# Performance work log

Hardware: AMD Instinct MI355X
Metric: run time of the kernel (lower is better)

Reference implementation:

```python
import jax, jax.numpy as jnp
import numpy as np

KS = 3          # deformable kernel size
PAD = 1         # padding (kernel_size // 2)
EPS = 1e-5      # BatchNorm eps


def conv2d(x, w, b):
    # plain 3x3 conv, stride 1, pad 1, NCHW / OIHW
    y = jax.lax.conv_general_dilated(x, w, window_strides=(1, 1),
                                     padding=[(PAD, PAD), (PAD, PAD)],
                                     dimension_numbers=("NCHW", "OIHW", "NCHW"))
    return y + b[None, :, None, None]


def deform_conv(x, offset, mask, w, b):
    # modulated deformable conv v2 (torchvision deform_conv2d semantics)
    B, C, H, W = x.shape
    K = KS * KS
    ky, kx = jnp.meshgrid(jnp.arange(KS), jnp.arange(KS), indexing="ij")
    ky = ky.reshape(-1).astype(x.dtype)
    kx = kx.reshape(-1).astype(x.dtype)
    off = offset.reshape(B, K, 2, H, W)          # channel order: (dy, dx) per kernel tap
    dy, dx = off[:, :, 0], off[:, :, 1]          # [B,K,H,W]
    py = dy + (ky - PAD)[None, :, None, None] + jnp.arange(H, dtype=x.dtype)[None, None, :, None]
    px = dx + (kx - PAD)[None, :, None, None] + jnp.arange(W, dtype=x.dtype)[None, None, None, :]
    y0 = jnp.floor(py); x0 = jnp.floor(px)
    ly = py - y0; lx = px - x0
    y0i = y0.astype(jnp.int32); x0i = x0.astype(jnp.int32)
    y1i = y0i + 1; x1i = x0i + 1
    xf = x.reshape(B, C, H * W)

    def gather(yi, xi):
        valid = (yi >= 0) & (yi < H) & (xi >= 0) & (xi < W)          # zero padding outside
        idx = jnp.clip(yi, 0, H - 1) * W + jnp.clip(xi, 0, W - 1)    # [B,K,H,W]
        g = jax.vmap(lambda xb, ib: jnp.take(xb, ib, axis=1))(xf, idx.reshape(B, -1))
        g = g.reshape(B, C, K, H, W)
        return g * valid[:, None].astype(x.dtype)

    v = (gather(y0i, x0i) * ((1 - ly) * (1 - lx))[:, None]
         + gather(y0i, x1i) * ((1 - ly) * lx)[:, None]
         + gather(y1i, x0i) * (ly * (1 - lx))[:, None]
         + gather(y1i, x1i) * (ly * lx)[:, None])                    # [B,C,K,H,W]
    v = v * mask[:, None]                                            # modulation
    out = jnp.einsum("bckhw,ock->bohw", v, w.reshape(w.shape[0], C, K))
    return out + b[None, :, None, None]


def setup_inputs() -> dict:
    key = jax.random.key(0)
    ks = jax.random.split(key, 5)
    B, Cin, Cout, H, W = 8, 64, 64, 128, 128
    K = KS * KS
    x = jax.random.normal(ks[0], (B, Cin, H, W), jnp.float32)
    off_w = jax.random.normal(ks[1], (2 * K, Cin, KS, KS), jnp.float32) * 0.01
    off_b = jnp.zeros((2 * K,), jnp.float32)
    mod_w = jax.random.normal(ks[2], (K, Cin, KS, KS), jnp.float32) * 0.01
    mod_b = jnp.zeros((K,), jnp.float32)
    w = jax.random.normal(ks[3], (Cout, Cin, KS, KS), jnp.float32) * (1.0 / np.sqrt(Cin * K))
    b = jnp.zeros((Cout,), jnp.float32)
    gamma = jnp.ones((Cout,), jnp.float32)
    beta = jnp.zeros((Cout,), jnp.float32)
    return {"x": x, "off_w": off_w, "off_b": off_b, "mod_w": mod_w,
            "mod_b": mod_b, "w": w, "b": b, "gamma": gamma, "beta": beta}


def reference(x, off_w, off_b, mod_w, mod_b, w, b, gamma, beta):
    offset = conv2d(x, off_w, off_b)                       # [B,2K,H,W]
    mask = 2.0 * jax.nn.sigmoid(conv2d(x, mod_w, mod_b))   # [B,K,H,W]
    y = deform_conv(x, offset, mask, w, b)                 # [B,Cout,H,W]
    # BatchNorm2d (training-mode batch stats, biased variance)
    mean = y.mean(axis=(0, 2, 3), keepdims=True)
    var = y.var(axis=(0, 2, 3), keepdims=True)
    yn = (y - mean) / jnp.sqrt(var + EPS)
    yn = gamma[None, :, None, None] * yn + beta[None, :, None, None]
    return jax.nn.relu(yn)
```

## Files before the change

### kernel.cpp

```cpp
#include <hip/hip_runtime.h>
#include <math.h>

#define Hn 128
#define Wn 128
#define HW 16384
#define NPIX 131072
#define EPSv 1e-5f

#define XT_OFF   0
#define OFF_OFF  4194304
#define MASK_OFF 6553600
#define WBTA_OFF 7733248
#define WBTB_OFF 7743488
#define STAT_OFF 7763968


typedef short s16x8 __attribute__((ext_vector_type(8)));
typedef unsigned short u16x4 __attribute__((ext_vector_type(4)));
typedef float f32x4 __attribute__((ext_vector_type(4)));

__device__ __forceinline__ unsigned short f2bf(float f) {
  unsigned u = __float_as_uint(f);
  return (unsigned short)((u + 0x7fffu + ((u >> 16) & 1u)) >> 16);
}
__device__ __forceinline__ float bf2f(unsigned short s) {
  return __uint_as_float((unsigned)s << 16);
}

__global__ __launch_bounds__(256) void prep_kernel(
    const float* __restrict__ off_w, const float* __restrict__ mod_w,
    const float* __restrict__ w, unsigned short* __restrict__ wbtA,
    unsigned short* __restrict__ wbtB, float* __restrict__ stat) {
  int i = blockIdx.x * 256 + threadIdx.x;
  if (i < 128) stat[i] = 0.f;
  if (i < 20480) {
    int e = i & 31, oc = (i >> 5) & 31, it = i >> 10;
    int tp = it % 5, chunk = it / 5;
    int tap = tp * 2 + (e >> 4);
    int c = (chunk << 4) + (e & 15);
    float v = 0.f;
    if (tap < 9) {
      if (oc < 18) v = off_w[(oc * 64 + c) * 9 + tap];
      else if (oc < 27) v = mod_w[((oc - 18) * 64 + c) * 9 + tap];
    }
    wbtA[i] = f2bf(v);
  } else if (i < 20480 + 40960) {
    int j = i - 20480;
    int j3 = j & 7;
    int l = (j >> 3) & 63;
    int nt = (j >> 9) & 3;
    int it = j >> 11;
    int tp = it % 5, chunk = it / 5;
    int tap = tp * 2 + (l >> 5);
    int c = (chunk << 4) + (((l >> 4) & 1) << 3) + j3;
    int oc = (nt << 4) + (l & 15);
    float v = (tap < 9) ? w[(oc * 64 + c) * 9 + tap] : 0.f;
    wbtB[j] = f2bf(v);
  }
}

__global__ __launch_bounds__(256) void xform_kernel(
    const float* __restrict__ x, unsigned short* __restrict__ xt) {
  int blk = blockIdx.x;
  int b = blk & 7;
  int hw = ((blk >> 3) << 8) + threadIdx.x;
  const float* xb = x + ((size_t)(b << 6) << 14) + hw;
  unsigned short* o = xt + (((size_t)(b << 14)) + hw) * 64;
#pragma unroll
  for (int g = 0; g < 8; ++g) {
    float v[8];
#pragma unroll
    for (int j = 0; j < 8; ++j) v[j] = xb[(size_t)((g << 3) + j) << 14];
    s16x8 pk;
#pragma unroll
    for (int j = 0; j < 8; ++j) pk[j] = (short)f2bf(v[j]);
    *(s16x8*)(o + (g << 3)) = pk;
  }
}

__global__ __launch_bounds__(256, 4) void convA_mfma_kernel(
    const unsigned short* __restrict__ xt, const unsigned short* __restrict__ wbtA,
    const float* __restrict__ off_b, const float* __restrict__ mod_b,
    float* __restrict__ off_out, float* __restrict__ mask_out) {
  int t = threadIdx.x;
  int bx = blockIdx.x;
  int b = bx & 7, h = bx >> 3;
  int ln = t & 15, quad = (t >> 4) & 3, wv = t >> 6;
  int p0 = (wv << 5) + ln, p1 = p0 + 16;
  int s_ = quad >> 1, cj = (quad & 1) << 3;

  f32x4 acc[2][2];
#pragma unroll
  for (int mt = 0; mt < 2; ++mt)
#pragma unroll
    for (int nt = 0; nt < 2; ++nt) acc[mt][nt] = (f32x4){0.f, 0.f, 0.f, 0.f};

  const unsigned short* xtb = xt + ((size_t)(b << 14)) * 64;

#pragma unroll 5
  for (int it = 0; it < 20; ++it) {
    int chunk = it / 5, tp = it - chunk * 5;
    int tap = tp * 2 + s_;
    s16x8 B0 = (s16x8){0, 0, 0, 0, 0, 0, 0, 0};
    s16x8 B1 = (s16x8){0, 0, 0, 0, 0, 0, 0, 0};
    if (tap < 9) {
      int gy = h + tap / 3 - 1;
      if (gy >= 0 && gy < Hn) {
        const unsigned short* rowp = xtb + ((size_t)(gy << 7)) * 64 + (chunk << 4) + cj;
        int gx0 = p0 + tap % 3 - 1;
        int gx1 = p1 + tap % 3 - 1;
        if (gx0 >= 0 && gx0 < Wn) B0 = *(const s16x8*)(rowp + (gx0 << 6));
        if (gx1 >= 0 && gx1 < Wn) B1 = *(const s16x8*)(rowp + (gx1 << 6));
      }
    }
#pragma unroll
    for (int mt = 0; mt < 2; ++mt) {
      s16x8 A = *(const s16x8*)(wbtA + (size_t)((it << 5) + (mt << 4) + ln) * 32 + (quad << 3));
      acc[mt][0] = __builtin_amdgcn_mfma_f32_16x16x32_bf16(A, B0, acc[mt][0], 0, 0, 0);
      acc[mt][1] = __builtin_amdgcn_mfma_f32_16x16x32_bf16(A, B1, acc[mt][1], 0, 0, 0);
    }
  }

  int hw = h << 7;
#pragma unroll
  for (int mt = 0; mt < 2; ++mt)
#pragma unroll
    for (int r = 0; r < 4; ++r) {
      int oc = (mt << 4) + (quad << 2) + r;
#pragma unroll
      for (int nt = 0; nt < 2; ++nt) {
        int px = (wv << 5) + (nt << 4) + ln;
        float val = acc[mt][nt][r];
        if (oc < 18) {
          off_out[(((size_t)b * 18 + oc) << 14) + hw + px] = val + off_b[oc];
        } else if (oc < 27) {
          float z = val + mod_b[oc - 18];
          mask_out[(((size_t)b * 9 + (oc - 18)) << 14) + hw + px] = 2.f / (1.f + expf(-z));
        }
      }
    }
}

__global__ __launch_bounds__(256, 4) void deform_mfma_kernel(
    const unsigned short* __restrict__ xt, const float* __restrict__ off,
    const float* __restrict__ mask, const unsigned short* __restrict__ wbtB,
    const float* __restrict__ bias, float* __restrict__ y) {
  __shared__ unsigned short geow[9 * 128 * 4];
  __shared__ unsigned short geoi[9 * 128];
  int t = threadIdx.x;
  int bx = blockIdx.x;
  int b = bx & 7, h = bx >> 3;
  int lane = t & 63, wv = t >> 6;
  int l4 = lane & 15;
  int s4 = lane >> 4;
  int tapS = lane >> 5;
  int chalf = s4 & 1;
  int hw = h << 7;

  for (int i = t; i < 1152; i += 256) {
    int tap = i >> 7, p2 = i & 127;
    int ob = ((b * 18 + 2 * tap) << 14) + hw + p2;
    float dy = off[ob];
    float dx = off[ob + HW];
    float m = mask[((b * 9 + tap) << 14) + hw + p2];
    float py = dy + (float)(h + tap / 3 - 1);
    float pxf = dx + (float)(p2 + tap % 3 - 1);
    float y0f = floorf(py), x0f = floorf(pxf);
    float ly = py - y0f, lx = pxf - x0f;
    int y0 = (int)y0f, x0 = (int)x0f;
    int y1 = y0 + 1, x1 = x0 + 1;
    float fy0 = (y0 >= 0 && y0 < Hn) ? 1.f : 0.f;
    float fy1 = (y1 >= 0 && y1 < Hn) ? 1.f : 0.f;
    float fx0 = (x0 >= 0 && x0 < Wn) ? 1.f : 0.f;
    float fx1 = (x1 >= 0 && x1 < Wn) ? 1.f : 0.f;
    float ax0 = (1.f - lx) * fx0, ax1 = lx * fx1;
    float ay0 = (1.f - ly) * fy0 * m, ay1 = ly * fy1 * m;
    int cy0 = min(max(y0, 0), Hn - 1), cy1 = min(max(y1, 0), Hn - 1);
    int cx0 = min(max(x0, 0), Wn - 1), cx1 = min(max(x1, 0), Wn - 1);
    int cbase = min(cx0, Wn - 2), rbase = min(cy0, Hn - 2);
    float gx0 = (cx0 == cbase ? ax0 : 0.f) + (cx1 == cbase ? ax1 : 0.f);
    float gx1 = (cx0 == cbase + 1 ? ax0 : 0.f) + (cx1 == cbase + 1 ? ax1 : 0.f);
    float gy0 = (cy0 == rbase ? ay0 : 0.f) + (cy1 == rbase ? ay1 : 0.f);
    float gy1 = (cy0 == rbase + 1 ? ay0 : 0.f) + (cy1 == rbase + 1 ? ay1 : 0.f);
    unsigned short* gw = geow + i * 4;
    gw[0] = f2bf(gy0);
    gw[1] = f2bf(gy1);
    gw[2] = f2bf(gx0);
    gw[3] = f2bf(gx1);
    geoi[i] = (unsigned short)((rbase << 7) + cbase);
  }
  __syncthreads();

  f32x4 acc[2][4];
#pragma unroll
  for (int m = 0; m < 2; ++m)
#pragma unroll
    for (int n = 0; n < 4; ++n) acc[m][n] = (f32x4){0.f, 0.f, 0.f, 0.f};

  const unsigned short* xtb = xt + ((size_t)(b << 14)) * 64;

  for (int tp = 0; tp < 5; ++tp) {
    int tap = tp * 2 + tapS;
    bool live = (tap < 9);
    float gy0[2], gy1[2], gx0[2], gx1[2];
    const unsigned short* cpb[2];
#pragma unroll
    for (int m = 0; m < 2; ++m) {
      if (live) {
        int px = (wv << 5) + (m << 4) + l4;
        int gidx = (tap << 7) + px;
        u16x4 wq = *(const u16x4*)(geow + gidx * 4);
        unsigned ib = geoi[gidx];
        gy0[m] = bf2f(wq[0]);
        gy1[m] = bf2f(wq[1]);
        gx0[m] = bf2f(wq[2]);
        gx1[m] = bf2f(wq[3]);
        cpb[m] = xtb + (size_t)ib * 64 + (chalf << 3);
      } else {
        cpb[m] = xtb;
        gy0[m] = gy1[m] = gx0[m] = gx1[m] = 0.f;
      }
    }
#pragma unroll 2
    for (int chunk = 0; chunk < 4; ++chunk) {
      int it = chunk * 5 + tp;
      s16x8 A[2];
#pragma unroll
      for (int m = 0; m < 2; ++m) {
        if (live) {
          const unsigned short* cp = cpb[m] + (chunk << 4);
          s16x8 c00 = *(const s16x8*)(cp);
          s16x8 c01 = *(const s16x8*)(cp + 64);
          s16x8 c10 = *(const s16x8*)(cp + 8192);
          s16x8 c11 = *(const s16x8*)(cp + 8192 + 64);
#pragma unroll
          for (int j = 0; j < 8; ++j) {
            float v = gy0[m] * (gx0[m] * bf2f((unsigned short)c00[j]) +
                                gx1[m] * bf2f((unsigned short)c01[j])) +
                      gy1[m] * (gx0[m] * bf2f((unsigned short)c10[j]) +
                                gx1[m] * bf2f((unsigned short)c11[j]));
            A[m][j] = (short)f2bf(v);
          }
        } else {
#pragma unroll
          for (int j = 0; j < 8; ++j) A[m][j] = 0;
        }
      }
      const unsigned short* wb = wbtB + (((size_t)it) << 11) + (lane << 3);
#pragma unroll
      for (int n = 0; n < 4; ++n) {
        s16x8 Bf = *(const s16x8*)(wb + (n << 9));
        acc[0][n] = __builtin_amdgcn_mfma_f32_16x16x32_bf16(A[0], Bf, acc[0][n], 0, 0, 0);
        acc[1][n] = __builtin_amdgcn_mfma_f32_16x16x32_bf16(A[1], Bf, acc[1][n], 0, 0, 0);
      }
    }
  }

#pragma unroll
  for (int m = 0; m < 2; ++m) {
    int px0 = (wv << 5) + (m << 4) + (s4 << 2);
#pragma unroll
    for (int n = 0; n < 4; ++n) {
      int oc = (n << 4) + l4;
      float bv = bias[oc];
      float4 o;
      o.x = acc[m][n][0] + bv;
      o.y = acc[m][n][1] + bv;
      o.z = acc[m][n][2] + bv;
      o.w = acc[m][n][3] + bv;
      *(float4*)(y + (((size_t)(b << 6) + oc) << 14) + hw + px0) = o;
    }
  }
}

__global__ __launch_bounds__(256) void stats2_kernel(
    const float* __restrict__ y, float* __restrict__ stat) {
  int bxx = blockIdx.x;
  int c = bxx & 63, sl = bxx >> 6;
  int bb = sl >> 1;
  const float4* yp = (const float4*)(y + (((size_t)bb * 64 + c) << 14) + ((sl & 1) << 13));
  float s = 0.f, ss = 0.f;
  for (int i = threadIdx.x; i < 2048; i += 256) {
    float4 v = yp[i];
    s += v.x + v.y + v.z + v.w;
    ss += v.x * v.x + v.y * v.y + v.z * v.z + v.w * v.w;
  }
#pragma unroll
  for (int o = 32; o > 0; o >>= 1) {
    s += __shfl_xor(s, o);
    ss += __shfl_xor(ss, o);
  }
  __shared__ float shs[4], shss[4];
  int lane = threadIdx.x & 63, wv = threadIdx.x >> 6;
  if (lane == 0) { shs[wv] = s; shss[wv] = ss; }
  __syncthreads();
  if (threadIdx.x == 0) {
    float S = shs[0] + shs[1] + shs[2] + shs[3];
    float SS = shss[0] + shss[1] + shss[2] + shss[3];
    atomicAdd(stat + c, S);
    atomicAdd(stat + 64 + c, SS);
  }
}

__global__ __launch_bounds__(256) void bnrelu_kernel(
    float* __restrict__ y, const float* __restrict__ stat,
    const float* __restrict__ gamma, const float* __restrict__ beta) {
  float4* y4 = (float4*)y;
  for (int i = blockIdx.x * 256 + threadIdx.x; i < 2097152; i += gridDim.x * 256) {
    int c = (i >> 12) & 63;
    float mean = stat[c] * (1.f / (float)NPIX);
    float var = stat[64 + c] * (1.f / (float)NPIX) - mean * mean;
    float r = rsqrtf(var + EPSv);
    float g = gamma[c] * r;
    float bt = beta[c] - mean * g;
    float4 v = y4[i];
    v.x = fmaxf(v.x * g + bt, 0.f);
    v.y = fmaxf(v.y * g + bt, 0.f);
    v.z = fmaxf(v.z * g + bt, 0.f);
    v.w = fmaxf(v.w * g + bt, 0.f);
    y4[i] = v;
  }
}

extern "C" void kernel_launch(void* const* d_in, const int* in_sizes, int n_in,
                              void* d_out, int out_size, void* d_ws, size_t ws_size,
                              hipStream_t stream) {
  const float* x     = (const float*)d_in[0];
  const float* off_w = (const float*)d_in[1];
  const float* off_b = (const float*)d_in[2];
  const float* mod_w = (const float*)d_in[3];
  const float* mod_b = (const float*)d_in[4];
  const float* w     = (const float*)d_in[5];
  const float* b     = (const float*)d_in[6];
  const float* gamma = (const float*)d_in[7];
  const float* beta  = (const float*)d_in[8];
  float* out = (float*)d_out;
  float* ws  = (float*)d_ws;

  unsigned short* xt  = (unsigned short*)(ws + XT_OFF);
  float* offo  = ws + OFF_OFF;
  float* masko = ws + MASK_OFF;
  unsigned short* wbtA = (unsigned short*)(ws + WBTA_OFF);
  unsigned short* wbtB = (unsigned short*)(ws + WBTB_OFF);
  float* stat  = ws + STAT_OFF;

  prep_kernel<<<240, 256, 0, stream>>>(off_w, mod_w, w, wbtA, wbtB, stat);
  xform_kernel<<<512, 256, 0, stream>>>(x, xt);
  convA_mfma_kernel<<<1024, 256, 0, stream>>>(xt, wbtA, off_b, mod_b, offo, masko);
  deform_mfma_kernel<<<1024, 256, 0, stream>>>(xt, offo, masko, wbtB, b, out);
  stats2_kernel<<<1024, 256, 0, stream>>>(out, stat);
  bnrelu_kernel<<<8192, 256, 0, stream>>>(out, stat, gamma, beta);
}
```

Measured before the change: 233.6 us.

## Split conv and deform kernels into half-row blocks and precombine bilinear weights

Both the offset/mask conv and the deformable conv kernels now cover half an image row per block. Each wave computes one 16-pixel tile instead of two, the grid doubles, and launch bounds ask for 8 waves per SIMD, which cuts register pressure and raises occupancy. The deform kernel also stores the four combined bilinear weights (gy*gx) in LDS and packs results with the hardware v_cvt_pk_bf16_f32 instruction, which reduces per-element ALU work. In exchange, A-operand reuse across two MFMA tiles is lost and the weights are loaded more often. Rounding the product weights to bf16 changes numerics slightly.

Measured after the change: 250.8 us. 7.4% more time.

```diff
diff --git a/kernel.cpp b/kernel.cpp
--- a/kernel.cpp
+++ b/kernel.cpp
@@ -18,6 +18,7 @@
 typedef short s16x8 __attribute__((ext_vector_type(8)));
 typedef unsigned short u16x4 __attribute__((ext_vector_type(4)));
 typedef float f32x4 __attribute__((ext_vector_type(4)));
+typedef unsigned int u32x4 __attribute__((ext_vector_type(4)));
 
 __device__ __forceinline__ unsigned short f2bf(float f) {
   unsigned u = __float_as_uint(f);
@@ -25,6 +26,11 @@
 }
 __device__ __forceinline__ float bf2f(unsigned short s) {
   return __uint_as_float((unsigned)s << 16);
+}
+__device__ __forceinline__ unsigned cvt_pk_bf16(float lo, float hi) {
+  unsigned r;
+  asm("v_cvt_pk_bf16_f32 %0, %1, %2" : "=v"(r) : "v"(lo), "v"(hi));
+  return r;
 }
 
 __global__ __launch_bounds__(256) void prep_kernel(
@@ -78,22 +84,20 @@
   }
 }
 
-__global__ __launch_bounds__(256, 4) void convA_mfma_kernel(
+__global__ __launch_bounds__(256, 8) void convA_mfma_kernel(
     const unsigned short* __restrict__ xt, const unsigned short* __restrict__ wbtA,
     const float* __restrict__ off_b, const float* __restrict__ mod_b,
     float* __restrict__ off_out, float* __restrict__ mask_out) {
   int t = threadIdx.x;
   int bx = blockIdx.x;
-  int b = bx & 7, h = bx >> 3;
+  int half = bx & 1, b = (bx >> 1) & 7, h = bx >> 4;
   int ln = t & 15, quad = (t >> 4) & 3, wv = t >> 6;
-  int p0 = (wv << 5) + ln, p1 = p0 + 16;
+  int p0 = (half << 6) + (wv << 4) + ln;
   int s_ = quad >> 1, cj = (quad & 1) << 3;
 
-  f32x4 acc[2][2];
-#pragma unroll
-  for (int mt = 0; mt < 2; ++mt)
-#pragma unroll
-    for (int nt = 0; nt < 2; ++nt) acc[mt][nt] = (f32x4){0.f, 0.f, 0.f, 0.f};
+  f32x4 acc[2];
+#pragma unroll
+  for (int mt = 0; mt < 2; ++mt) acc[mt] = (f32x4){0.f, 0.f, 0.f, 0.f};
 
   const unsigned short* xtb = xt + ((size_t)(b << 14)) * 64;
 
@@ -102,22 +106,18 @@
     int chunk = it / 5, tp = it - chunk * 5;
     int tap = tp * 2 + s_;
     s16x8 B0 = (s16x8){0, 0, 0, 0, 0, 0, 0, 0};
-    s16x8 B1 = (s16x8){0, 0, 0, 0, 0, 0, 0, 0};
     if (tap < 9) {
       int gy = h + tap / 3 - 1;
       if (gy >= 0 && gy < Hn) {
         const unsigned short* rowp = xtb + ((size_t)(gy << 7)) * 64 + (chunk << 4) + cj;
         int gx0 = p0 + tap % 3 - 1;
-        int gx1 = p1 + tap % 3 - 1;
         if (gx0 >= 0 && gx0 < Wn) B0 = *(const s16x8*)(rowp + (gx0 << 6));
-        if (gx1 >= 0 && gx1 < Wn) B1 = *(const s16x8*)(rowp + (gx1 << 6));
       }
     }
 #pragma unroll
     for (int mt = 0; mt < 2; ++mt) {
       s16x8 A = *(const s16x8*)(wbtA + (size_t)((it << 5) + (mt << 4) + ln) * 32 + (quad << 3));
-      acc[mt][0] = __builtin_amdgcn_mfma_f32_16x16x32_bf16(A, B0, acc[mt][0], 0, 0, 0);
-      acc[mt][1] = __builtin_amdgcn_mfma_f32_16x16x32_bf16(A, B1, acc[mt][1], 0, 0, 0);
+      acc[mt] = __builtin_amdgcn_mfma_f32_16x16x32_bf16(A, B0, acc[mt], 0, 0, 0);
     }
   }
 
@@ -127,44 +127,43 @@
 #pragma unroll
     for (int r = 0; r < 4; ++r) {
       int oc = (mt << 4) + (quad << 2) + r;
-#pragma unroll
-      for (int nt = 0; nt < 2; ++nt) {
-        int px = (wv << 5) + (nt << 4) + ln;
-        float val = acc[mt][nt][r];
-        if (oc < 18) {
-          off_out[(((size_t)b * 18 + oc) << 14) + hw + px] = val + off_b[oc];
-        } else if (oc < 27) {
-          float z = val + mod_b[oc - 18];
-          mask_out[(((size_t)b * 9 + (oc - 18)) << 14) + hw + px] = 2.f / (1.f + expf(-z));
-        }
+      int px = p0;
+      float val = acc[mt][r];
+      if (oc < 18) {
+        off_out[(((size_t)b * 18 + oc) << 14) + hw + px] = val + off_b[oc];
+      } else if (oc < 27) {
+        float z = val + mod_b[oc - 18];
+        mask_out[(((size_t)b * 9 + (oc - 18)) << 14) + hw + px] = 2.f / (1.f + expf(-z));
       }
     }
 }
 
-__global__ __launch_bounds__(256, 4) void deform_mfma_kernel(
+__global__ __launch_bounds__(256, 8) void deform_mfma_kernel(
     const unsigned short* __restrict__ xt, const float* __restrict__ off,
     const float* __restrict__ mask, const unsigned short* __restrict__ wbtB,
     const float* __restrict__ bias, float* __restrict__ y) {
-  __shared__ unsigned short geow[9 * 128 * 4];
-  __shared__ unsigned short geoi[9 * 128];
+  __shared__ unsigned short geow[9 * 64 * 4];
+  __shared__ unsigned short geoi[9 * 64];
   int t = threadIdx.x;
   int bx = blockIdx.x;
-  int b = bx & 7, h = bx >> 3;
+  int half = bx & 1, b = (bx >> 1) & 7, h = bx >> 4;
   int lane = t & 63, wv = t >> 6;
   int l4 = lane & 15;
   int s4 = lane >> 4;
   int tapS = lane >> 5;
   int chalf = s4 & 1;
   int hw = h << 7;
-
-  for (int i = t; i < 1152; i += 256) {
-    int tap = i >> 7, p2 = i & 127;
-    int ob = ((b * 18 + 2 * tap) << 14) + hw + p2;
+  int pxb = half << 6;
+
+  for (int i = t; i < 576; i += 256) {
+    int tap = i >> 6, p2 = i & 63;
+    int px = pxb + p2;
+    int ob = ((b * 18 + 2 * tap) << 14) + hw + px;
     float dy = off[ob];
     float dx = off[ob + HW];
-    float m = mask[((b * 9 + tap) << 14) + hw + p2];
+    float m = mask[((b * 9 + tap) << 14) + hw + px];
     float py = dy + (float)(h + tap / 3 - 1);
-    float pxf = dx + (float)(p2 + tap % 3 - 1);
+    float pxf = dx + (float)(px + tap % 3 - 1);
     float y0f = floorf(py), x0f = floorf(pxf);
     float ly = py - y0f, lx = pxf - x0f;
     int y0 = (int)y0f, x0 = (int)x0f;
@@ -183,93 +182,82 @@
     float gy0 = (cy0 == rbase ? ay0 : 0.f) + (cy1 == rbase ? ay1 : 0.f);
     float gy1 = (cy0 == rbase + 1 ? ay0 : 0.f) + (cy1 == rbase + 1 ? ay1 : 0.f);
     unsigned short* gw = geow + i * 4;
-    gw[0] = f2bf(gy0);
-    gw[1] = f2bf(gy1);
-    gw[2] = f2bf(gx0);
-    gw[3] = f2bf(gx1);
+    gw[0] = f2bf(gy0 * gx0);
+    gw[1] = f2bf(gy0 * gx1);
+    gw[2] = f2bf(gy1 * gx0);
+    gw[3] = f2bf(gy1 * gx1);
     geoi[i] = (unsigned short)((rbase << 7) + cbase);
   }
   __syncthreads();
 
-  f32x4 acc[2][4];
-#pragma unroll
-  for (int m = 0; m < 2; ++m)
-#pragma unroll
-    for (int n = 0; n < 4; ++n) acc[m][n] = (f32x4){0.f, 0.f, 0.f, 0.f};
+  f32x4 acc[4];
+#pragma unroll
+  for (int n = 0; n < 4; ++n) acc[n] = (f32x4){0.f, 0.f, 0.f, 0.f};
 
   const unsigned short* xtb = xt + ((size_t)(b << 14)) * 64;
 
   for (int tp = 0; tp < 5; ++tp) {
     int tap = tp * 2 + tapS;
     bool live = (tap < 9);
-    float gy0[2], gy1[2], gx0[2], gx1[2];
-    const unsigned short* cpb[2];
-#pragma unroll
-    for (int m = 0; m < 2; ++m) {
-      if (live) {
-        int px = (wv << 5) + (m << 4) + l4;
-        int gidx = (tap << 7) + px;
-        u16x4 wq = *(const u16x4*)(geow + gidx * 4);
-        unsigned ib = geoi[gidx];
-        gy0[m] = bf2f(wq[0]);
-        gy1[m] = bf2f(wq[1]);
-        gx0[m] = bf2f(wq[2]);
-        gx1[m] = bf2f(wq[3]);
-        cpb[m] = xtb + (size_t)ib * 64 + (chalf << 3);
-      } else {
-        cpb[m] = xtb;
-        gy0[m] = gy1[m] = gx0[m] = gx1[m] = 0.f;
-      }
-    }
-#pragma unroll 2
+    float w00, w01, w10, w11;
+    const unsigned short* cpb;
+    if (live) {
+      int gidx = (tap << 6) + (wv << 4) + l4;
+      u16x4 wq = *(const u16x4*)(geow + gidx * 4);
+      unsigned ib = geoi[gidx];
+      w00 = bf2f(wq[0]);
+      w01 = bf2f(wq[1]);
+      w10 = bf2f(wq[2]);
+      w11 = bf2f(wq[3]);
+      cpb = xtb + (size_t)ib * 64 + (chalf << 3);
+    } else {
+      cpb = xtb;
+      w00 = w01 = w10 = w11 = 0.f;
+    }
+#pragma unroll
     for (int chunk = 0; chunk < 4; ++chunk) {
       int it = chunk * 5 + tp;
-      s16x8 A[2];
-#pragma unroll
-      for (int m = 0; m < 2; ++m) {
-        if (live) {
-          const unsigned short* cp = cpb[m] + (chunk << 4);
-          s16x8 c00 = *(const s16x8*)(cp);
-          s16x8 c01 = *(const s16x8*)(cp + 64);
-          s16x8 c10 = *(const s16x8*)(cp + 8192);
-          s16x8 c11 = *(const s16x8*)(cp + 8192 + 64);
-#pragma unroll
-          for (int j = 0; j < 8; ++j) {
-            float v = gy0[m] * (gx0[m] * bf2f((unsigned short)c00[j]) +
-                                gx1[m] * bf2f((unsigned short)c01[j])) +
-                      gy1[m] * (gx0[m] * bf2f((unsigned short)c10[j]) +
-                                gx1[m] * bf2f((unsigned short)c11[j]));
-            A[m][j] = (short)f2bf(v);
-          }
-        } else {
-#pragma unroll
-          for (int j = 0; j < 8; ++j) A[m][j] = 0;
+      u32x4 au = (u32x4){0u, 0u, 0u, 0u};
+      if (live) {
+        const unsigned short* cp = cpb + (chunk << 4);
+        s16x8 c00 = *(const s16x8*)(cp);
+        s16x8 c01 = *(const s16x8*)(cp + 64);
+        s16x8 c10 = *(const s16x8*)(cp + 8192);
+        s16x8 c11 = *(const s16x8*)(cp + 8192 + 64);
+#pragma unroll
+        for (int jj = 0; jj < 4; ++jj) {
+          float v0 = w00 * bf2f((unsigned short)c00[2 * jj]) +
+                     w01 * bf2f((unsigned short)c01[2 * jj]) +
+                     w10 * bf2f((unsigned short)c10[2 * jj]) +
+                     w11 * bf2f((unsigned short)c11[2 * jj]);
+          float v1 = w00 * bf2f((unsigned short)c00[2 * jj + 1]) +
+                     w01 * bf2f((unsigned short)c01[2 * jj + 1]) +
+                     w10 * bf2f((unsigned short)c10[2 * jj + 1]) +
+                     w11 * bf2f((unsigned short)c11[2 * jj + 1]);
+          au[jj] = cvt_pk_bf16(v0, v1);
         }
       }
+      s16x8 A = __builtin_bit_cast(s16x8, au);
       const unsigned short* wb = wbtB + (((size_t)it) << 11) + (lane << 3);
 #pragma unroll
       for (int n = 0; n < 4; ++n) {
         s16x8 Bf = *(const s16x8*)(wb + (n << 9));
-        acc[0][n] = __builtin_amdgcn_mfma_f32_16x16x32_bf16(A[0], Bf, acc[0][n], 0, 0, 0);
-        acc[1][n] = __builtin_amdgcn_mfma_f32_16x16x32_bf16(A[1], Bf, acc[1][n], 0, 0, 0);
+        acc[n] = __builtin_amdgcn_mfma_f32_16x16x32_bf16(A, Bf, acc[n], 0, 0, 0);
       }
     }
   }
 
-#pragma unroll
-  for (int m = 0; m < 2; ++m) {
-    int px0 = (wv << 5) + (m << 4) + (s4 << 2);
-#pragma unroll
-    for (int n = 0; n < 4; ++n) {
-      int oc = (n << 4) + l4;
-      float bv = bias[oc];
-      float4 o;
-      o.x = acc[m][n][0] + bv;
-      o.y = acc[m][n][1] + bv;
-      o.z = acc[m][n][2] + bv;
-      o.w = acc[m][n][3] + bv;
-      *(float4*)(y + (((size_t)(b << 6) + oc) << 14) + hw + px0) = o;
-    }
+  int px0 = pxb + (wv << 4) + (s4 << 2);
+#pragma unroll
+  for (int n = 0; n < 4; ++n) {
+    int oc = (n << 4) + l4;
+    float bv = bias[oc];
+    float4 o;
+    o.x = acc[n][0] + bv;
+    o.y = acc[n][1] + bv;
+    o.z = acc[n][2] + bv;
+    o.w = acc[n][3] + bv;
+    *(float4*)(y + (((size_t)(b << 6) + oc) << 14) + hw + px0) = o;
   }
 }
 
@@ -346,8 +334,8 @@
 
   prep_kernel<<<240, 256, 0, stream>>>(off_w, mod_w, w, wbtA, wbtB, stat);
   xform_kernel<<<512, 256, 0, stream>>>(x, xt);
-  convA_mfma_kernel<<<1024, 256, 0, stream>>>(xt, wbtA, off_b, mod_b, offo, masko);
-  deform_mfma_kernel<<<1024, 256, 0, stream>>>(xt, offo, masko, wbtB, b, out);
+  convA_mfma_kernel<<<2048, 256, 0, stream>>>(xt, wbtA, off_b, mod_b, offo, masko);
+  deform_mfma_kernel<<<2048, 256, 0, stream>>>(xt, offo, masko, wbtB, b, out);
   stats2_kernel<<<1024, 256, 0, stream>>>(out, stat);
   bnrelu_kernel<<<8192, 256, 0, stream>>>(out, stat, gamma, beta);
 }
```

## Fuse offset/mask conv into deformable conv kernel via shared memory

Applied to the files above, without the earlier changes.

Merges the offset/mask convolution kernel into the deformable convolution kernel. Each block computes its row's offsets and sigmoid mask into shared memory, so the global write and re-read of the offset/mask tensors and one launch go away. It also precomputes the four combined bilinear weights per sample and packs the bf16 conversion with v_cvt_pk_bf16_f32, which cuts per-element ALU work in the gather loop. In exchange the fused kernel uses more shared memory (about 13.8KB extra) and more registers, which may lower occupancy, and folding the weights before the bf16 rounding slightly changes numerics.

After: 230.1 us. Within noise of the previous version (-1.5%).

```diff
diff --git a/kernel.cpp b/kernel.cpp
--- a/kernel.cpp
+++ b/kernel.cpp
@@ -8,16 +8,15 @@
 #define EPSv 1e-5f
 
 #define XT_OFF   0
-#define OFF_OFF  4194304
-#define MASK_OFF 6553600
-#define WBTA_OFF 7733248
-#define WBTB_OFF 7743488
-#define STAT_OFF 7763968
+#define WBTA_OFF 4194304
+#define WBTB_OFF 4204544
+#define STAT_OFF 4225024
 
 
 typedef short s16x8 __attribute__((ext_vector_type(8)));
 typedef unsigned short u16x4 __attribute__((ext_vector_type(4)));
 typedef float f32x4 __attribute__((ext_vector_type(4)));
+typedef unsigned int u32x4 __attribute__((ext_vector_type(4)));
 
 __device__ __forceinline__ unsigned short f2bf(float f) {
   unsigned u = __float_as_uint(f);
@@ -25,6 +24,11 @@
 }
 __device__ __forceinline__ float bf2f(unsigned short s) {
   return __uint_as_float((unsigned)s << 16);
+}
+__device__ __forceinline__ unsigned cvt_pk_bf16(float lo, float hi) {
+  unsigned r;
+  asm("v_cvt_pk_bf16_f32 %0, %1, %2" : "=v"(r) : "v"(lo), "v"(hi));
+  return r;
 }
 
 __global__ __launch_bounds__(256) void prep_kernel(
@@ -78,91 +82,81 @@
   }
 }
 
-__global__ __launch_bounds__(256, 4) void convA_mfma_kernel(
+__global__ __launch_bounds__(256, 4) void fused_dconv_kernel(
     const unsigned short* __restrict__ xt, const unsigned short* __restrict__ wbtA,
+    const unsigned short* __restrict__ wbtB,
     const float* __restrict__ off_b, const float* __restrict__ mod_b,
-    float* __restrict__ off_out, float* __restrict__ mask_out) {
-  int t = threadIdx.x;
-  int bx = blockIdx.x;
-  int b = bx & 7, h = bx >> 3;
-  int ln = t & 15, quad = (t >> 4) & 3, wv = t >> 6;
-  int p0 = (wv << 5) + ln, p1 = p0 + 16;
-  int s_ = quad >> 1, cj = (quad & 1) << 3;
-
-  f32x4 acc[2][2];
-#pragma unroll
-  for (int mt = 0; mt < 2; ++mt)
-#pragma unroll
-    for (int nt = 0; nt < 2; ++nt) acc[mt][nt] = (f32x4){0.f, 0.f, 0.f, 0.f};
-
-  const unsigned short* xtb = xt + ((size_t)(b << 14)) * 64;
-
-#pragma unroll 5
-  for (int it = 0; it < 20; ++it) {
-    int chunk = it / 5, tp = it - chunk * 5;
-    int tap = tp * 2 + s_;
-    s16x8 B0 = (s16x8){0, 0, 0, 0, 0, 0, 0, 0};
-    s16x8 B1 = (s16x8){0, 0, 0, 0, 0, 0, 0, 0};
-    if (tap < 9) {
-      int gy = h + tap / 3 - 1;
-      if (gy >= 0 && gy < Hn) {
-        const unsigned short* rowp = xtb + ((size_t)(gy << 7)) * 64 + (chunk << 4) + cj;
-        int gx0 = p0 + tap % 3 - 1;
-        int gx1 = p1 + tap % 3 - 1;
-        if (gx0 >= 0 && gx0 < Wn) B0 = *(const s16x8*)(rowp + (gx0 << 6));
-        if (gx1 >= 0 && gx1 < Wn) B1 = *(const s16x8*)(rowp + (gx1 << 6));
-      }
-    }
-#pragma unroll
-    for (int mt = 0; mt < 2; ++mt) {
-      s16x8 A = *(const s16x8*)(wbtA + (size_t)((it << 5) + (mt << 4) + ln) * 32 + (quad << 3));
-      acc[mt][0] = __builtin_amdgcn_mfma_f32_16x16x32_bf16(A, B0, acc[mt][0], 0, 0, 0);
-      acc[mt][1] = __builtin_amdgcn_mfma_f32_16x16x32_bf16(A, B1, acc[mt][1], 0, 0, 0);
-    }
-  }
-
-  int hw = h << 7;
-#pragma unroll
-  for (int mt = 0; mt < 2; ++mt)
-#pragma unroll
-    for (int r = 0; r < 4; ++r) {
-      int oc = (mt << 4) + (quad << 2) + r;
-#pragma unroll
-      for (int nt = 0; nt < 2; ++nt) {
-        int px = (wv << 5) + (nt << 4) + ln;
-        float val = acc[mt][nt][r];
-        if (oc < 18) {
-          off_out[(((size_t)b * 18 + oc) << 14) + hw + px] = val + off_b[oc];
-        } else if (oc < 27) {
-          float z = val + mod_b[oc - 18];
-          mask_out[(((size_t)b * 9 + (oc - 18)) << 14) + hw + px] = 2.f / (1.f + expf(-z));
-        }
-      }
-    }
-}
-
-__global__ __launch_bounds__(256, 4) void deform_mfma_kernel(
-    const unsigned short* __restrict__ xt, const float* __restrict__ off,
-    const float* __restrict__ mask, const unsigned short* __restrict__ wbtB,
     const float* __restrict__ bias, float* __restrict__ y) {
+  __shared__ float offm[27 * 128];
   __shared__ unsigned short geow[9 * 128 * 4];
   __shared__ unsigned short geoi[9 * 128];
   int t = threadIdx.x;
   int bx = blockIdx.x;
   int b = bx & 7, h = bx >> 3;
   int lane = t & 63, wv = t >> 6;
-  int l4 = lane & 15;
-  int s4 = lane >> 4;
-  int tapS = lane >> 5;
-  int chalf = s4 & 1;
+  int ln = lane & 15, quad = (lane >> 4) & 3;
   int hw = h << 7;
+
+  const unsigned short* xtb = xt + ((size_t)(b << 14)) * 64;
+
+  {
+    int p0 = (wv << 5) + ln, p1 = p0 + 16;
+    int s_ = quad >> 1, cj = (quad & 1) << 3;
+    f32x4 acc[2][2];
+#pragma unroll
+    for (int mt = 0; mt < 2; ++mt)
+#pragma unroll
+      for (int nt = 0; nt < 2; ++nt) acc[mt][nt] = (f32x4){0.f, 0.f, 0.f, 0.f};
+
+#pragma unroll 5
+    for (int it = 0; it < 20; ++it) {
+      int chunk = it / 5, tp = it - chunk * 5;
+      int tap = tp * 2 + s_;
+      s16x8 B0 = (s16x8){0, 0, 0, 0, 0, 0, 0, 0};
+      s16x8 B1 = (s16x8){0, 0, 0, 0, 0, 0, 0, 0};
+      if (tap < 9) {
+        int gy = h + tap / 3 - 1;
+        if (gy >= 0 && gy < Hn) {
+          const unsigned short* rowp = xtb + ((size_t)(gy << 7)) * 64 + (chunk << 4) + cj;
+          int gx0 = p0 + tap % 3 - 1;
+          int gx1 = p1 + tap % 3 - 1;
+          if (gx0 >= 0 && gx0 < Wn) B0 = *(const s16x8*)(rowp + (gx0 << 6));
+          if (gx1 >= 0 && gx1 < Wn) B1 = *(const s16x8*)(rowp + (gx1 << 6));
+        }
+      }
+#pragma unroll
+      for (int mt = 0; mt < 2; ++mt) {
+        s16x8 A = *(const s16x8*)(wbtA + (size_t)((it << 5) + (mt << 4) + ln) * 32 + (quad << 3));
+        acc[mt][0] = __builtin_amdgcn_mfma_f32_16x16x32_bf16(A, B0, acc[mt][0], 0, 0, 0);
+        acc[mt][1] = __builtin_amdgcn_mfma_f32_16x16x32_bf16(A, B1, acc[mt][1], 0, 0, 0);
+      }
+    }
+
+#pragma unroll
+    for (int mt = 0; mt < 2; ++mt)
+#pragma unroll
+      for (int r = 0; r < 4; ++r) {
+        int oc = (mt << 4) + (quad << 2) + r;
+#pragma unroll
+        for (int nt = 0; nt < 2; ++nt) {
+          int px = (wv << 5) + (nt << 4) + ln;
+          float val = acc[mt][nt][r];
+          if (oc < 18) {
+            offm[(oc << 7) + px] = val + off_b[oc];
+          } else if (oc < 27) {
+            float z = val + mod_b[oc - 18];
+            offm[(oc << 7) + px] = 2.f / (1.f + expf(-z));
+          }
+        }
+      }
+  }
+  __syncthreads();
 
   for (int i = t; i < 1152; i += 256) {
     int tap = i >> 7, p2 = i & 127;
-    int ob = ((b * 18 + 2 * tap) << 14) + hw + p2;
-    float dy = off[ob];
-    float dx = off[ob + HW];
-    float m = mask[((b * 9 + tap) << 14) + hw + p2];
+    float dy = offm[((2 * tap) << 7) + p2];
+    float dx = offm[((2 * tap + 1) << 7) + p2];
+    float m = offm[((18 + tap) << 7) + p2];
     float py = dy + (float)(h + tap / 3 - 1);
     float pxf = dx + (float)(p2 + tap % 3 - 1);
     float y0f = floorf(py), x0f = floorf(pxf);
@@ -183,26 +177,29 @@
     float gy0 = (cy0 == rbase ? ay0 : 0.f) + (cy1 == rbase ? ay1 : 0.f);
     float gy1 = (cy0 == rbase + 1 ? ay0 : 0.f) + (cy1 == rbase + 1 ? ay1 : 0.f);
     unsigned short* gw = geow + i * 4;
-    gw[0] = f2bf(gy0);
-    gw[1] = f2bf(gy1);
-    gw[2] = f2bf(gx0);
-    gw[3] = f2bf(gx1);
+    gw[0] = f2bf(gy0 * gx0);
+    gw[1] = f2bf(gy0 * gx1);
+    gw[2] = f2bf(gy1 * gx0);
+    gw[3] = f2bf(gy1 * gx1);
     geoi[i] = (unsigned short)((rbase << 7) + cbase);
   }
   __syncthreads();
 
+  int l4 = ln;
+  int s4 = lane >> 4;
+  int tapS = lane >> 5;
+  int chalf = s4 & 1;
+
   f32x4 acc[2][4];
 #pragma unroll
   for (int m = 0; m < 2; ++m)
 #pragma unroll
     for (int n = 0; n < 4; ++n) acc[m][n] = (f32x4){0.f, 0.f, 0.f, 0.f};
-
-  const unsigned short* xtb = xt + ((size_t)(b << 14)) * 64;
 
   for (int tp = 0; tp < 5; ++tp) {
     int tap = tp * 2 + tapS;
     bool live = (tap < 9);
-    float gy0[2], gy1[2], gx0[2], gx1[2];
+    float w00[2], w01[2], w10[2], w11[2];
     const unsigned short* cpb[2];
 #pragma unroll
     for (int m = 0; m < 2; ++m) {
@@ -211,14 +208,14 @@
         int gidx = (tap << 7) + px;
         u16x4 wq = *(const u16x4*)(geow + gidx * 4);
         unsigned ib = geoi[gidx];
-        gy0[m] = bf2f(wq[0]);
-        gy1[m] = bf2f(wq[1]);
-        gx0[m] = bf2f(wq[2]);
-        gx1[m] = bf2f(wq[3]);
+        w00[m] = bf2f(wq[0]);
+        w01[m] = bf2f(wq[1]);
+        w10[m] = bf2f(wq[2]);
+        w11[m] = bf2f(wq[3]);
         cpb[m] = xtb + (size_t)ib * 64 + (chalf << 3);
       } else {
         cpb[m] = xtb;
-        gy0[m] = gy1[m] = gx0[m] = gx1[m] = 0.f;
+        w00[m] = w01[m] = w10[m] = w11[m] = 0.f;
       }
     }
 #pragma unroll 2
@@ -233,17 +230,22 @@
           s16x8 c01 = *(const s16x8*)(cp + 64);
           s16x8 c10 = *(const s16x8*)(cp + 8192);
           s16x8 c11 = *(const s16x8*)(cp + 8192 + 64);
-#pragma unroll
-          for (int j = 0; j < 8; ++j) {
-            float v = gy0[m] * (gx0[m] * bf2f((unsigned short)c00[j]) +
-                                gx1[m] * bf2f((unsigned short)c01[j])) +
-                      gy1[m] * (gx0[m] * bf2f((unsigned short)c10[j]) +
-                                gx1[m] * bf2f((unsigned short)c11[j]));
-            A[m][j] = (short)f2bf(v);
+          u32x4 au;
+#pragma unroll
+          for (int jj = 0; jj < 4; ++jj) {
+            float v0 = w00[m] * bf2f((unsigned short)c00[2 * jj]) +
+                       w01[m] * bf2f((unsigned short)c01[2 * jj]) +
+                       w10[m] * bf2f((unsigned short)c10[2 * jj]) +
+                       w11[m] * bf2f((unsigned short)c11[2 * jj]);
+            float v1 = w00[m] * bf2f((unsigned short)c00[2 * jj + 1]) +
+                       w01[m] * bf2f((unsigned short)c01[2 * jj + 1]) +
+                       w10[m] * bf2f((unsigned short)c10[2 * jj + 1]) +
+                       w11[m] * bf2f((unsigned short)c11[2 * jj + 1]);
+            au[jj] = cvt_pk_bf16(v0, v1);
           }
+          A[m] = __builtin_bit_cast(s16x8, au);
         } else {
-#pragma unroll
-          for (int j = 0; j < 8; ++j) A[m][j] = 0;
+          A[m] = (s16x8){0, 0, 0, 0, 0, 0, 0, 0};
         }
       }
       const unsigned short* wb = wbtB + (((size_t)it) << 11) + (lane << 3);
@@ -338,16 +340,13 @@
   float* ws  = (float*)d_ws;
 
   unsigned short* xt  = (unsigned short*)(ws + XT_OFF);
-  float* offo  = ws + OFF_OFF;
-  float* masko = ws + MASK_OFF;
   unsigned short* wbtA = (unsigned short*)(ws + WBTA_OFF);
   unsigned short* wbtB = (unsigned short*)(ws + WBTB_OFF);
   float* stat  = ws + STAT_OFF;
 
   prep_kernel<<<240, 256, 0, stream>>>(off_w, mod_w, w, wbtA, wbtB, stat);
   xform_kernel<<<512, 256, 0, stream>>>(x, xt);
-  convA_mfma_kernel<<<1024, 256, 0, stream>>>(xt, wbtA, off_b, mod_b, offo, masko);
-  deform_mfma_kernel<<<1024, 256, 0, stream>>>(xt, offo, masko, wbtB, b, out);
+  fused_dconv_kernel<<<1024, 256, 0, stream>>>(xt, wbtA, wbtB, off_b, mod_b, b, out);
   stats2_kernel<<<1024, 256, 0, stream>>>(out, stat);
   bnrelu_kernel<<<8192, 256, 0, stream>>>(out, stat, gamma, beta);
 }
```
